# Performance work log

Measured on AMD Instinct MI355X. Metric: run time of the kernel, lower is better.

Reference implementation:

```python
import jax, jax.numpy as jnp
import numpy as np

N_NODES = 50000
N_EDGES = 800000
IN_FEATS = 128
OUT_FEATS = 128


def setup_inputs() -> dict:
    key = jax.random.key(0)
    k1, k2, k3, k4 = jax.random.split(key, 4)
    x = jax.random.normal(k1, (N_NODES, IN_FEATS), dtype=jnp.float32)
    src = jax.random.randint(k2, (N_EDGES,), 0, N_NODES, dtype=jnp.int32)
    dst = jax.random.randint(k3, (N_EDGES,), 0, N_NODES, dtype=jnp.int32)
    # xavier_uniform init for weight [in_feats, out_feats]
    limit = float(np.sqrt(6.0 / (IN_FEATS + OUT_FEATS)))
    weight = jax.random.uniform(k4, (IN_FEATS, OUT_FEATS), dtype=jnp.float32,
                                minval=-limit, maxval=limit)
    bias = jnp.zeros((OUT_FEATS,), dtype=jnp.float32)
    return {"x": x, "src": src, "dst": dst, "weight": weight, "bias": bias}


def reference(x, src, dst, weight, bias):
    # GraphConv, norm='both', no edge_weight (copy_u path), single partition:
    #   x <- x * out_deg^{-1/2}
    #   h[v] = sum_{(u->v) in E} x[u]            (SpMM aggregation)
    #   rst = h @ W                               (GEMM)
    #   rst <- rst * in_deg^{-1/2} + bias
    n = x.shape[0]
    ones = jnp.ones(src.shape[0], dtype=x.dtype)
    deg_out = jax.ops.segment_sum(ones, src, num_segments=n)     # [N]
    deg_out = jnp.maximum(deg_out, 1.0)[:, None]                  # clamp(min=1)
    xn = x * jax.lax.rsqrt(deg_out)                               # left norm
    h = jax.ops.segment_sum(xn[src], dst, num_segments=n)        # [N, in]
    rst = h @ weight                                              # [N, out]
    deg_in = jax.ops.segment_sum(ones, dst, num_segments=n)      # [N]
    deg_in = jnp.maximum(deg_in, 1.0)[:, None]
    rst = rst * jax.lax.rsqrt(deg_in)                             # right norm
    return rst + bias
```

## Files before the change

### kernel.cpp

```cpp
#include <hip/hip_runtime.h>

#define F 128
#define RANGE 12500
#define WT_LD 136

typedef unsigned short ushort_t;
typedef unsigned char uchar_t;
typedef _Float16 half8 __attribute__((ext_vector_type(8)));
typedef float f32x4 __attribute__((ext_vector_type(4)));

__device__ inline float bf_lo(unsigned u) { return __uint_as_float(u << 16); }
__device__ inline float bf_hi(unsigned u) { return __uint_as_float(u & 0xffff0000u); }
__device__ inline ushort_t f2bf(float f) {
    unsigned u = __float_as_uint(f);
    return (ushort_t)((u + 0x7fff + ((u >> 16) & 1)) >> 16);
}

__device__ __forceinline__
void gemm_body(_Float16* Wt, const float* __restrict__ x, const float* __restrict__ W,
               ushort_t* __restrict__ Y, int N, int gb) {
    const int t = threadIdx.x;
    for (int i = t; i < 128 * 128; i += 1024) {
        int k = i >> 7, c = i & 127;
        Wt[c * WT_LD + k] = (_Float16)W[i];
    }
    __syncthreads();

    const int wv = t >> 6;
    const int l  = t & 63;
    const int m  = l & 15;
    const int q  = l >> 4;
    const int r0w = gb * 256 + wv * 16;
    const int rowload = min(r0w + m, N - 1);
    const float* xr = x + (size_t)rowload * F;

    f32x4 acc[8] = {};
    #pragma unroll
    for (int k0 = 0; k0 < 128; k0 += 32) {
        const int kk = k0 + q * 8;
        float4 xa = *(const float4*)(xr + kk);
        float4 xb = *(const float4*)(xr + kk + 4);
        half8 a;
        a[0] = (_Float16)xa.x; a[1] = (_Float16)xa.y;
        a[2] = (_Float16)xa.z; a[3] = (_Float16)xa.w;
        a[4] = (_Float16)xb.x; a[5] = (_Float16)xb.y;
        a[6] = (_Float16)xb.z; a[7] = (_Float16)xb.w;
        #pragma unroll
        for (int ct = 0; ct < 8; ++ct) {
            half8 bfr = *(const half8*)&Wt[(ct * 16 + m) * WT_LD + kk];
            acc[ct] = __builtin_amdgcn_mfma_f32_16x16x32_f16(a, bfr, acc[ct], 0, 0, 0);
        }
    }

    #pragma unroll
    for (int ct = 0; ct < 8; ++ct) {
        #pragma unroll
        for (int reg = 0; reg < 4; ++reg) {
            int rr = r0w + q * 4 + reg;
            if (rr < N) Y[(size_t)rr * F + ct * 16 + m] = f2bf(acc[ct][reg]);
        }
    }
}

__global__ __launch_bounds__(1024)
void hist_gemm_kernel(const int* __restrict__ src, const int* __restrict__ dst,
                      ushort_t* __restrict__ part, int E, int S, int SLICE,
                      const float* __restrict__ x, const float* __restrict__ W,
                      ushort_t* __restrict__ Y, int N, int HB) {
    __shared__ union {
        int h[RANGE];
        _Float16 Wt[128 * WT_LD];
    } sm;
    int b = blockIdx.x, t = threadIdx.x;

    if (b >= HB) { gemm_body(sm.Wt, x, W, Y, N, b - HB); return; }

    int r = b / S, s = b % S;
    int lo = r * RANGE;
    for (int i = t; i < RANGE; i += 1024) sm.h[i] = 0;
    __syncthreads();
    int e0 = s * SLICE, e1 = min(e0 + SLICE, E);
    int e = e0 + t * 4;
    for (; e + 3 < e1; e += 4096) {
        int4 vs4 = *(const int4*)(src + e);
        int4 vd4 = *(const int4*)(dst + e);
        int vs, vd;
        vs = vs4.x - lo; if ((unsigned)vs < (unsigned)RANGE) atomicAdd(&sm.h[vs], 1);
        vs = vs4.y - lo; if ((unsigned)vs < (unsigned)RANGE) atomicAdd(&sm.h[vs], 1);
        vs = vs4.z - lo; if ((unsigned)vs < (unsigned)RANGE) atomicAdd(&sm.h[vs], 1);
        vs = vs4.w - lo; if ((unsigned)vs < (unsigned)RANGE) atomicAdd(&sm.h[vs], 1);
        vd = vd4.x - lo; if ((unsigned)vd < (unsigned)RANGE) atomicAdd(&sm.h[vd], 0x10000);
        vd = vd4.y - lo; if ((unsigned)vd < (unsigned)RANGE) atomicAdd(&sm.h[vd], 0x10000);
        vd = vd4.z - lo; if ((unsigned)vd < (unsigned)RANGE) atomicAdd(&sm.h[vd], 0x10000);
        vd = vd4.w - lo; if ((unsigned)vd < (unsigned)RANGE) atomicAdd(&sm.h[vd], 0x10000);
    }
    for (; e < e1; ++e) {
        int vs = src[e] - lo;
        int vd = dst[e] - lo;
        if ((unsigned)vs < (unsigned)RANGE) atomicAdd(&sm.h[vs], 1);
        if ((unsigned)vd < (unsigned)RANGE) atomicAdd(&sm.h[vd], 0x10000);
    }
    __syncthreads();
    ushort_t* outp = part + (size_t)b * RANGE;
    for (int i = t; i < RANGE; i += 1024) {
        int hv = sm.h[i];
        outp[i] = (ushort_t)((hv & 0xff) | ((hv >> 8) & 0xff00));
    }
}

__global__ __launch_bounds__(256)
void reduce_all_kernel(const ushort_t* __restrict__ part, uchar_t* __restrict__ pre8,
                       float* __restrict__ inv_out, int* __restrict__ cnt_in,
                       int* __restrict__ psum, int S, int N) {
    int b = blockIdx.x, t = threadIdx.x;
    int v = b * 256 + t;
    int run = 0;
    if (v < N) {
        int r = v / RANGE, vp = v % RANGE;
        const ushort_t* p = part + (size_t)r * S * RANGE + vp;
        uchar_t* q = pre8 + (size_t)r * S * RANGE + vp;
        int sum_s = 0;
        #pragma unroll 8
        for (int s = 0; s < S; ++s) {
            int tv = p[(size_t)s * RANGE];
            sum_s += tv & 0xff;
            q[(size_t)s * RANGE] = (uchar_t)run;
            run += (tv >> 8);
        }
        inv_out[v] = rsqrtf(fmaxf((float)sum_s, 1.0f));
        cnt_in[v] = run;
    }
    int bl = run;
    #pragma unroll
    for (int off = 32; off > 0; off >>= 1) bl += __shfl_down(bl, off);
    __shared__ int ws[4];
    int lane = t & 63, w = t >> 6;
    if (lane == 0) ws[w] = bl;
    __syncthreads();
    if (t == 0) psum[b] = ws[0] + ws[1] + ws[2] + ws[3];
}

__global__ __launch_bounds__(256)
void scan_rows_kernel(const int* __restrict__ cnt_in, const int* __restrict__ psum,
                      int* __restrict__ row_off, int N, int E, int NP) {
    int b = blockIdx.x, t = threadIdx.x;
    int pv = (t < 4 * b && t < NP) ? psum[t] : 0;
    #pragma unroll
    for (int off = 32; off > 0; off >>= 1) pv += __shfl_down(pv, off);
    __shared__ int red[4];
    int lane = t & 63, w = t >> 6;
    if (lane == 0) red[w] = pv;
    if (b == 0 && t == 0) row_off[N] = E;
    __syncthreads();
    int base = red[0] + red[1] + red[2] + red[3];

    int i0 = b * 1024 + t * 4;
    int v[4]; int s = 0;
    #pragma unroll
    for (int j = 0; j < 4; ++j) { int i = i0 + j; v[j] = (i < N) ? cnt_in[i] : 0; s += v[j]; }
    int incl = s;
    #pragma unroll
    for (int off = 1; off < 64; off <<= 1) {
        int u = __shfl_up(incl, off);
        if (lane >= off) incl += u;
    }
    __shared__ int wsum[4];
    if (lane == 63) wsum[w] = incl;
    __syncthreads();
    int wbase = 0;
    #pragma unroll
    for (int j = 0; j < 4; ++j) if (j < w) wbase += wsum[j];
    int run = base + wbase + (incl - s);
    #pragma unroll
    for (int j = 0; j < 4; ++j) {
        int i = i0 + j;
        if (i < N) { row_off[i] = run; run += v[j]; }
    }
}

__global__ __launch_bounds__(1024)
void fill_gemm_kernel(const int* __restrict__ src, const int* __restrict__ dst,
                      const int* __restrict__ row_off, const uchar_t* __restrict__ pre8,
                      ushort_t* __restrict__ csr_src,
                      const float* __restrict__ x, const float* __restrict__ W,
                      ushort_t* __restrict__ Y,
                      int E, int S, int SLICE, int N, int FB, int G1) {
    __shared__ union {
        int cur[RANGE];
        _Float16 Wt[128 * WT_LD];
    } sm;
    const int t = threadIdx.x;
    const int blk = blockIdx.x;

    if (blk >= FB) { gemm_body(sm.Wt, x, W, Y, N, G1 + (blk - FB)); return; }

    int r = blk / S, s = blk % S;
    int lo = r * RANGE;
    int hi = min(lo + RANGE, N);
    const uchar_t* pp = pre8 + (size_t)blk * RANGE;
    for (int i = t; i < hi - lo; i += 1024) sm.cur[i] = row_off[lo + i] + pp[i];
    __syncthreads();
    int e0 = s * SLICE, e1 = min(e0 + SLICE, E);
    int e = e0 + t * 4;
    for (; e + 3 < e1; e += 4096) {
        int4 vd4 = *(const int4*)(dst + e);
        int4 vs4 = *(const int4*)(src + e);
        int d;
        d = vd4.x - lo; if ((unsigned)d < (unsigned)(hi - lo)) { int pos = atomicAdd(&sm.cur[d], 1); csr_src[pos] = (ushort_t)vs4.x; }
        d = vd4.y - lo; if ((unsigned)d < (unsigned)(hi - lo)) { int pos = atomicAdd(&sm.cur[d], 1); csr_src[pos] = (ushort_t)vs4.y; }
        d = vd4.z - lo; if ((unsigned)d < (unsigned)(hi - lo)) { int pos = atomicAdd(&sm.cur[d], 1); csr_src[pos] = (ushort_t)vs4.z; }
        d = vd4.w - lo; if ((unsigned)d < (unsigned)(hi - lo)) { int pos = atomicAdd(&sm.cur[d], 1); csr_src[pos] = (ushort_t)vs4.w; }
    }
    for (; e < e1; ++e) {
        int d = dst[e] - lo;
        if ((unsigned)d < (unsigned)(hi - lo)) {
            int pos = atomicAdd(&sm.cur[d], 1);
            csr_src[pos] = (ushort_t)src[e];
        }
    }
}

__global__ __launch_bounds__(256)
void gather_kernel(const ushort_t* __restrict__ Y, const ushort_t* __restrict__ csr_src,
                   const int* __restrict__ row_off, const float* __restrict__ inv_out,
                   const float* __restrict__ bias, float* __restrict__ out, int N) {
    int v = blockIdx.x * 4 + (threadIdx.x >> 6);
    if (v >= N) return;
    int lane = threadIdx.x & 63;
    int q = lane >> 4;
    int l16 = lane & 15;
    int beg = row_off[v], end = row_off[v + 1];
    float aA[8] = {0,0,0,0,0,0,0,0};
    float aB[8] = {0,0,0,0,0,0,0,0};
    float aC[8] = {0,0,0,0,0,0,0,0};
    float aD[8] = {0,0,0,0,0,0,0,0};
    int j = beg + q;
    for (; j + 12 < end; j += 16) {
        int s0 = csr_src[j];
        int s1 = csr_src[j + 4];
        int s2 = csr_src[j + 8];
        int s3 = csr_src[j + 12];
        float iv0 = inv_out[s0];
        float iv1 = inv_out[s1];
        float iv2 = inv_out[s2];
        float iv3 = inv_out[s3];
        uint4 u0 = *(const uint4*)(Y + (size_t)s0 * F + l16 * 8);
        uint4 u1 = *(const uint4*)(Y + (size_t)s1 * F + l16 * 8);
        uint4 u2 = *(const uint4*)(Y + (size_t)s2 * F + l16 * 8);
        uint4 u3 = *(const uint4*)(Y + (size_t)s3 * F + l16 * 8);
        aA[0] += bf_lo(u0.x) * iv0; aA[1] += bf_hi(u0.x) * iv0;
        aA[2] += bf_lo(u0.y) * iv0; aA[3] += bf_hi(u0.y) * iv0;
        aA[4] += bf_lo(u0.z) * iv0; aA[5] += bf_hi(u0.z) * iv0;
        aA[6] += bf_lo(u0.w) * iv0; aA[7] += bf_hi(u0.w) * iv0;
        aB[0] += bf_lo(u1.x) * iv1; aB[1] += bf_hi(u1.x) * iv1;
        aB[2] += bf_lo(u1.y) * iv1; aB[3] += bf_hi(u1.y) * iv1;
        aB[4] += bf_lo(u1.z) * iv1; aB[5] += bf_hi(u1.z) * iv1;
        aB[6] += bf_lo(u1.w) * iv1; aB[7] += bf_hi(u1.w) * iv1;
        aC[0] += bf_lo(u2.x) * iv2; aC[1] += bf_hi(u2.x) * iv2;
        aC[2] += bf_lo(u2.y) * iv2; aC[3] += bf_hi(u2.y) * iv2;
        aC[4] += bf_lo(u2.z) * iv2; aC[5] += bf_hi(u2.z) * iv2;
        aC[6] += bf_lo(u2.w) * iv2; aC[7] += bf_hi(u2.w) * iv2;
        aD[0] += bf_lo(u3.x) * iv3; aD[1] += bf_hi(u3.x) * iv3;
        aD[2] += bf_lo(u3.y) * iv3; aD[3] += bf_hi(u3.y) * iv3;
        aD[4] += bf_lo(u3.z) * iv3; aD[5] += bf_hi(u3.z) * iv3;
        aD[6] += bf_lo(u3.w) * iv3; aD[7] += bf_hi(u3.w) * iv3;
    }
    if (j < end) {
        int s0 = csr_src[j];
        float iv0 = inv_out[s0];
        uint4 u0 = *(const uint4*)(Y + (size_t)s0 * F + l16 * 8);
        aA[0] += bf_lo(u0.x) * iv0; aA[1] += bf_hi(u0.x) * iv0;
        aA[2] += bf_lo(u0.y) * iv0; aA[3] += bf_hi(u0.y) * iv0;
        aA[4] += bf_lo(u0.z) * iv0; aA[5] += bf_hi(u0.z) * iv0;
        aA[6] += bf_lo(u0.w) * iv0; aA[7] += bf_hi(u0.w) * iv0;
    }
    if (j + 4 < end) {
        int s1 = csr_src[j + 4];
        float iv1 = inv_out[s1];
        uint4 u1 = *(const uint4*)(Y + (size_t)s1 * F + l16 * 8);
        aB[0] += bf_lo(u1.x) * iv1; aB[1] += bf_hi(u1.x) * iv1;
        aB[2] += bf_lo(u1.y) * iv1; aB[3] += bf_hi(u1.y) * iv1;
        aB[4] += bf_lo(u1.z) * iv1; aB[5] += bf_hi(u1.z) * iv1;
        aB[6] += bf_lo(u1.w) * iv1; aB[7] += bf_hi(u1.w) * iv1;
    }
    if (j + 8 < end) {
        int s2 = csr_src[j + 8];
        float iv2 = inv_out[s2];
        uint4 u2 = *(const uint4*)(Y + (size_t)s2 * F + l16 * 8);
        aC[0] += bf_lo(u2.x) * iv2; aC[1] += bf_hi(u2.x) * iv2;
        aC[2] += bf_lo(u2.y) * iv2; aC[3] += bf_hi(u2.y) * iv2;
        aC[4] += bf_lo(u2.z) * iv2; aC[5] += bf_hi(u2.z) * iv2;
        aC[6] += bf_lo(u2.w) * iv2; aC[7] += bf_hi(u2.w) * iv2;
    }
    #pragma unroll
    for (int i = 0; i < 8; ++i) {
        float a = (aA[i] + aB[i]) + (aC[i] + aD[i]);
        a += __shfl_xor(a, 16);
        a += __shfl_xor(a, 32);
        aA[i] = a;
    }
    if (q == 0) {
        float invd = rsqrtf(fmaxf((float)(end - beg), 1.0f));
        float4 b0 = *(const float4*)(bias + l16 * 8);
        float4 b1 = *(const float4*)(bias + l16 * 8 + 4);
        float4 o0, o1;
        o0.x = aA[0] * invd + b0.x; o0.y = aA[1] * invd + b0.y;
        o0.z = aA[2] * invd + b0.z; o0.w = aA[3] * invd + b0.w;
        o1.x = aA[4] * invd + b1.x; o1.y = aA[5] * invd + b1.y;
        o1.z = aA[6] * invd + b1.z; o1.w = aA[7] * invd + b1.w;
        *(float4*)(out + (size_t)v * F + l16 * 8) = o0;
        *(float4*)(out + (size_t)v * F + l16 * 8 + 4) = o1;
    }
}

extern "C" void kernel_launch(void* const* d_in, const int* in_sizes, int n_in,
                              void* d_out, int out_size, void* d_ws, size_t ws_size,
                              hipStream_t stream) {
    const float* x    = (const float*)d_in[0];
    const int*   src  = (const int*)d_in[1];
    const int*   dst  = (const int*)d_in[2];
    const float* W    = (const float*)d_in[3];
    const float* bias = (const float*)d_in[4];
    float* out = (float*)d_out;

    const int N = in_sizes[0] / F;
    const int E = in_sizes[1];
    const int NB = (N + 1023) / 1024;
    const int NP = (N + 255) / 256;
    const int R = (N + RANGE - 1) / RANGE;

    size_t fixed_bytes = (size_t)N * 4
                       + (size_t)(N + 1) * 4
                       + (size_t)N * 4
                       + (size_t)NP * 4 + 256
                       + (size_t)E * 2 + 256
                       + (size_t)N * F * 2 + 256;
    int S = 64;
    while (S > 2 && fixed_bytes + (size_t)R * S * RANGE * 3 > ws_size) S >>= 1;
    const int SLICE = (E + S - 1) / S;
    const size_t K = (size_t)R * S * RANGE;

    char* base = (char*)d_ws;
    int*   cnt_in  = (int*)base;
    int*   row_off = cnt_in + N;
    float* inv_out = (float*)(row_off + N + 1);
    int*   psum    = (int*)(inv_out + N);
    size_t o1 = (((size_t)NP * 4 + (size_t)(3 * N + 1) * 4) + 255) & ~(size_t)255;
    ushort_t* csr_src = (ushort_t*)(base + o1);
    size_t o2 = (o1 + (size_t)E * 2 + 255) & ~(size_t)255;
    ushort_t* Y    = (ushort_t*)(base + o2);
    size_t o3 = (o2 + (size_t)N * F * 2 + 255) & ~(size_t)255;
    ushort_t* part = (ushort_t*)(base + o3);
    size_t o4 = (o3 + K * 2 + 255) & ~(size_t)255;
    uchar_t* pre8  = (uchar_t*)(base + o4);

    const int hgrid = R * S;
    const int GB = (N + 255) / 256;
    const int G1 = GB / 2;
    const int G2 = GB - G1;

    hist_gemm_kernel<<<hgrid + G1, 1024, 0, stream>>>(src, dst, part, E, S, SLICE,
                                                      x, W, Y, N, hgrid);
    reduce_all_kernel<<<NP, 256, 0, stream>>>(part, pre8, inv_out, cnt_in, psum, S, N);
    scan_rows_kernel<<<NB, 256, 0, stream>>>(cnt_in, psum, row_off, N, E, NP);
    fill_gemm_kernel<<<hgrid + G2, 1024, 0, stream>>>(src, dst, row_off, pre8, csr_src,
                                                      x, W, Y, E, S, SLICE, N, hgrid, G1);
    gather_kernel<<<(N + 3) / 4, 256, 0, stream>>>(Y, csr_src, row_off, inv_out,
                                                   bias, out, N);
}
```

Before: 152.0 us.

## Pack degree and cursor counters into sub-word fields to cut edge passes

The histogram kernel now packs two nodes into each shared int using 8-bit source and destination counts. That doubles the node range per block and halves the number of range passes over the edge list. The fill kernel keeps byte-wide cursors, four per int, covering all nodes in one block, so each edge slice is read once instead of once per node range. Per-edge row_off and pre8 lookups now come from global memory, and the layout assumes at most 255 edges per node per slice and a node count that fits the fixed 12500-word shared array.

```diff
diff --git a/kernel.cpp b/kernel.cpp
--- a/kernel.cpp
+++ b/kernel.cpp
@@ -1,7 +1,7 @@
 #include <hip/hip_runtime.h>
 
 #define F 128
-#define RANGE 12500
+#define RANGE_H 25000
 #define WT_LD 136
 
 typedef unsigned short ushort_t;
@@ -68,7 +68,7 @@
                       const float* __restrict__ x, const float* __restrict__ W,
                       ushort_t* __restrict__ Y, int N, int HB) {
     __shared__ union {
-        int h[RANGE];
+        int h[RANGE_H / 2];
         _Float16 Wt[128 * WT_LD];
     } sm;
     int b = blockIdx.x, t = threadIdx.x;
@@ -76,36 +76,33 @@
     if (b >= HB) { gemm_body(sm.Wt, x, W, Y, N, b - HB); return; }
 
     int r = b / S, s = b % S;
-    int lo = r * RANGE;
-    for (int i = t; i < RANGE; i += 1024) sm.h[i] = 0;
+    int lo = r * RANGE_H;
+    for (int i = t; i < RANGE_H / 2; i += 1024) sm.h[i] = 0;
     __syncthreads();
     int e0 = s * SLICE, e1 = min(e0 + SLICE, E);
     int e = e0 + t * 4;
     for (; e + 3 < e1; e += 4096) {
         int4 vs4 = *(const int4*)(src + e);
         int4 vd4 = *(const int4*)(dst + e);
-        int vs, vd;
-        vs = vs4.x - lo; if ((unsigned)vs < (unsigned)RANGE) atomicAdd(&sm.h[vs], 1);
-        vs = vs4.y - lo; if ((unsigned)vs < (unsigned)RANGE) atomicAdd(&sm.h[vs], 1);
-        vs = vs4.z - lo; if ((unsigned)vs < (unsigned)RANGE) atomicAdd(&sm.h[vs], 1);
-        vs = vs4.w - lo; if ((unsigned)vs < (unsigned)RANGE) atomicAdd(&sm.h[vs], 1);
-        vd = vd4.x - lo; if ((unsigned)vd < (unsigned)RANGE) atomicAdd(&sm.h[vd], 0x10000);
-        vd = vd4.y - lo; if ((unsigned)vd < (unsigned)RANGE) atomicAdd(&sm.h[vd], 0x10000);
-        vd = vd4.z - lo; if ((unsigned)vd < (unsigned)RANGE) atomicAdd(&sm.h[vd], 0x10000);
-        vd = vd4.w - lo; if ((unsigned)vd < (unsigned)RANGE) atomicAdd(&sm.h[vd], 0x10000);
+        int v;
+        v = vs4.x - lo; if ((unsigned)v < (unsigned)RANGE_H) atomicAdd(&sm.h[v >> 1], 1 << ((v & 1) * 16));
+        v = vs4.y - lo; if ((unsigned)v < (unsigned)RANGE_H) atomicAdd(&sm.h[v >> 1], 1 << ((v & 1) * 16));
+        v = vs4.z - lo; if ((unsigned)v < (unsigned)RANGE_H) atomicAdd(&sm.h[v >> 1], 1 << ((v & 1) * 16));
+        v = vs4.w - lo; if ((unsigned)v < (unsigned)RANGE_H) atomicAdd(&sm.h[v >> 1], 1 << ((v & 1) * 16));
+        v = vd4.x - lo; if ((unsigned)v < (unsigned)RANGE_H) atomicAdd(&sm.h[v >> 1], 0x100 << ((v & 1) * 16));
+        v = vd4.y - lo; if ((unsigned)v < (unsigned)RANGE_H) atomicAdd(&sm.h[v >> 1], 0x100 << ((v & 1) * 16));
+        v = vd4.z - lo; if ((unsigned)v < (unsigned)RANGE_H) atomicAdd(&sm.h[v >> 1], 0x100 << ((v & 1) * 16));
+        v = vd4.w - lo; if ((unsigned)v < (unsigned)RANGE_H) atomicAdd(&sm.h[v >> 1], 0x100 << ((v & 1) * 16));
     }
     for (; e < e1; ++e) {
         int vs = src[e] - lo;
         int vd = dst[e] - lo;
-        if ((unsigned)vs < (unsigned)RANGE) atomicAdd(&sm.h[vs], 1);
-        if ((unsigned)vd < (unsigned)RANGE) atomicAdd(&sm.h[vd], 0x10000);
-    }
-    __syncthreads();
-    ushort_t* outp = part + (size_t)b * RANGE;
-    for (int i = t; i < RANGE; i += 1024) {
-        int hv = sm.h[i];
-        outp[i] = (ushort_t)((hv & 0xff) | ((hv >> 8) & 0xff00));
-    }
+        if ((unsigned)vs < (unsigned)RANGE_H) atomicAdd(&sm.h[vs >> 1], 1 << ((vs & 1) * 16));
+        if ((unsigned)vd < (unsigned)RANGE_H) atomicAdd(&sm.h[vd >> 1], 0x100 << ((vd & 1) * 16));
+    }
+    __syncthreads();
+    int* outp = (int*)(part + (size_t)b * RANGE_H);
+    for (int i = t; i < RANGE_H / 2; i += 1024) outp[i] = sm.h[i];
 }
 
 __global__ __launch_bounds__(256)
@@ -116,15 +113,15 @@
     int v = b * 256 + t;
     int run = 0;
     if (v < N) {
-        int r = v / RANGE, vp = v % RANGE;
-        const ushort_t* p = part + (size_t)r * S * RANGE + vp;
-        uchar_t* q = pre8 + (size_t)r * S * RANGE + vp;
+        int rh = v / RANGE_H, vph = v % RANGE_H;
+        const ushort_t* p = part + (size_t)rh * S * RANGE_H + vph;
+        uchar_t* q = pre8 + v;
         int sum_s = 0;
         #pragma unroll 8
         for (int s = 0; s < S; ++s) {
-            int tv = p[(size_t)s * RANGE];
+            int tv = p[(size_t)s * RANGE_H];
             sum_s += tv & 0xff;
-            q[(size_t)s * RANGE] = (uchar_t)run;
+            q[(size_t)s * N] = (uchar_t)run;
             run += (tv >> 8);
         }
         inv_out[v] = rsqrtf(fmaxf((float)sum_s, 1.0f));
@@ -186,7 +183,7 @@
                       ushort_t* __restrict__ Y,
                       int E, int S, int SLICE, int N, int FB, int G1) {
     __shared__ union {
-        int cur[RANGE];
+        int cur4[12500];
         _Float16 Wt[128 * WT_LD];
     } sm;
     const int t = threadIdx.x;
@@ -194,29 +191,35 @@
 
     if (blk >= FB) { gemm_body(sm.Wt, x, W, Y, N, G1 + (blk - FB)); return; }
 
-    int r = blk / S, s = blk % S;
-    int lo = r * RANGE;
-    int hi = min(lo + RANGE, N);
-    const uchar_t* pp = pre8 + (size_t)blk * RANGE;
-    for (int i = t; i < hi - lo; i += 1024) sm.cur[i] = row_off[lo + i] + pp[i];
-    __syncthreads();
-    int e0 = s * SLICE, e1 = min(e0 + SLICE, E);
+    const int nw = (N + 3) >> 2;
+    for (int i = t; i < nw; i += 1024) sm.cur4[i] = 0;
+    __syncthreads();
+    const uchar_t* pp = pre8 + (size_t)blk * N;
+    int e0 = blk * SLICE, e1 = min(e0 + SLICE, E);
     int e = e0 + t * 4;
     for (; e + 3 < e1; e += 4096) {
         int4 vd4 = *(const int4*)(dst + e);
         int4 vs4 = *(const int4*)(src + e);
-        int d;
-        d = vd4.x - lo; if ((unsigned)d < (unsigned)(hi - lo)) { int pos = atomicAdd(&sm.cur[d], 1); csr_src[pos] = (ushort_t)vs4.x; }
-        d = vd4.y - lo; if ((unsigned)d < (unsigned)(hi - lo)) { int pos = atomicAdd(&sm.cur[d], 1); csr_src[pos] = (ushort_t)vs4.y; }
-        d = vd4.z - lo; if ((unsigned)d < (unsigned)(hi - lo)) { int pos = atomicAdd(&sm.cur[d], 1); csr_src[pos] = (ushort_t)vs4.z; }
-        d = vd4.w - lo; if ((unsigned)d < (unsigned)(hi - lo)) { int pos = atomicAdd(&sm.cur[d], 1); csr_src[pos] = (ushort_t)vs4.w; }
+        int d, sh, rel, pos;
+        d = vd4.x; sh = (d & 3) * 8;
+        rel = (atomicAdd(&sm.cur4[d >> 2], 1u << sh) >> sh) & 0xff;
+        pos = row_off[d] + pp[d] + rel; csr_src[pos] = (ushort_t)vs4.x;
+        d = vd4.y; sh = (d & 3) * 8;
+        rel = (atomicAdd(&sm.cur4[d >> 2], 1u << sh) >> sh) & 0xff;
+        pos = row_off[d] + pp[d] + rel; csr_src[pos] = (ushort_t)vs4.y;
+        d = vd4.z; sh = (d & 3) * 8;
+        rel = (atomicAdd(&sm.cur4[d >> 2], 1u << sh) >> sh) & 0xff;
+        pos = row_off[d] + pp[d] + rel; csr_src[pos] = (ushort_t)vs4.z;
+        d = vd4.w; sh = (d & 3) * 8;
+        rel = (atomicAdd(&sm.cur4[d >> 2], 1u << sh) >> sh) & 0xff;
+        pos = row_off[d] + pp[d] + rel; csr_src[pos] = (ushort_t)vs4.w;
     }
     for (; e < e1; ++e) {
-        int d = dst[e] - lo;
-        if ((unsigned)d < (unsigned)(hi - lo)) {
-            int pos = atomicAdd(&sm.cur[d], 1);
-            csr_src[pos] = (ushort_t)src[e];
-        }
+        int d = dst[e];
+        int sh = (d & 3) * 8;
+        int rel = (atomicAdd(&sm.cur4[d >> 2], 1u << sh) >> sh) & 0xff;
+        int pos = row_off[d] + pp[d] + rel;
+        csr_src[pos] = (ushort_t)src[e];
     }
 }
 
@@ -327,7 +330,7 @@
     const int E = in_sizes[1];
     const int NB = (N + 1023) / 1024;
     const int NP = (N + 255) / 256;
-    const int R = (N + RANGE - 1) / RANGE;
+    const int RH = (N + RANGE_H - 1) / RANGE_H;
 
     size_t fixed_bytes = (size_t)N * 4
                        + (size_t)(N + 1) * 4
@@ -336,9 +339,10 @@
                        + (size_t)E * 2 + 256
                        + (size_t)N * F * 2 + 256;
     int S = 64;
-    while (S > 2 && fixed_bytes + (size_t)R * S * RANGE * 3 > ws_size) S >>= 1;
+    while (S > 2 && fixed_bytes + (size_t)RH * S * RANGE_H * 2 + (size_t)S * N > ws_size)
+        S >>= 1;
     const int SLICE = (E + S - 1) / S;
-    const size_t K = (size_t)R * S * RANGE;
+    const size_t KH = (size_t)RH * S * RANGE_H;
 
     char* base = (char*)d_ws;
     int*   cnt_in  = (int*)base;
@@ -351,10 +355,11 @@
     ushort_t* Y    = (ushort_t*)(base + o2);
     size_t o3 = (o2 + (size_t)N * F * 2 + 255) & ~(size_t)255;
     ushort_t* part = (ushort_t*)(base + o3);
-    size_t o4 = (o3 + K * 2 + 255) & ~(size_t)255;
+    size_t o4 = (o3 + KH * 2 + 255) & ~(size_t)255;
     uchar_t* pre8  = (uchar_t*)(base + o4);
 
-    const int hgrid = R * S;
+    const int hgrid = RH * S;
+    const int fgrid = S;
     const int GB = (N + 255) / 256;
     const int G1 = GB / 2;
     const int G2 = GB - G1;
@@ -363,8 +368,8 @@
                                                       x, W, Y, N, hgrid);
     reduce_all_kernel<<<NP, 256, 0, stream>>>(part, pre8, inv_out, cnt_in, psum, S, N);
     scan_rows_kernel<<<NB, 256, 0, stream>>>(cnt_in, psum, row_off, N, E, NP);
-    fill_gemm_kernel<<<hgrid + G2, 1024, 0, stream>>>(src, dst, row_off, pre8, csr_src,
-                                                      x, W, Y, E, S, SLICE, N, hgrid, G1);
+    fill_gemm_kernel<<<fgrid + G2, 1024, 0, stream>>>(src, dst, row_off, pre8, csr_src,
+                                                      x, W, Y, E, S, SLICE, N, fgrid, G1);
     gather_kernel<<<(N + 3) / 4, 256, 0, stream>>>(Y, csr_src, row_off, inv_out,
                                                    bias, out, N);
 }
```

Result: slower. 164.4 us (+8.1%).
